# Kernel tuning notes

Hardware: AMD Instinct MI355X
Metric: run time of the kernel (lower is better)

Reference implementation:

```python
import jax, jax.numpy as jnp
import numpy as np

B, T, D, K = 64, 4096, 90, 32
LOG2PI = 1.8378770664093453


def setup_inputs() -> dict:
    key = jax.random.key(0)
    k1, k2, k3, k4, k5 = jax.random.split(key, 5)
    X = jax.random.normal(k1, (B, T, D), dtype=jnp.float32)
    state_priors = jax.random.uniform(k2, (K,), dtype=jnp.float32)
    transition_matrix = jax.random.uniform(k3, (K, K), dtype=jnp.float32)
    mu = jax.random.normal(k4, (K, D), dtype=jnp.float32) * 0.5
    log_var = jax.random.normal(k5, (K, D), dtype=jnp.float32) * 0.1
    return {"X": X, "state_priors": state_priors,
            "transition_matrix": transition_matrix, "mu": mu, "log_var": log_var}


def _emission_logprobs(X, mu, log_var):
    # Diagonal-Gaussian log density per state: (B,T,K)
    # expand (x-mu)^2*inv_var to avoid materializing a (B,T,K,D) tensor
    inv_var = jnp.exp(-log_var)                                   # (K,D)
    quad = (jnp.einsum('btd,kd->btk', X * X, inv_var)
            - 2.0 * jnp.einsum('btd,kd->btk', X, mu * inv_var)
            + jnp.sum(mu * mu * inv_var, axis=-1))                # (B,T,K)
    return -0.5 * (quad + jnp.sum(log_var, axis=-1) + D * LOG2PI)


def reference(X, state_priors, transition_matrix, mu, log_var):
    log_A = jax.nn.log_softmax(transition_matrix, axis=1)   # (K,K)
    log_pi = jax.nn.log_softmax(state_priors, axis=0)       # (K,)
    em = _emission_logprobs(X, mu, log_var)                 # (B,T,K)

    log_alpha0 = log_pi + em[:, 0, :]                       # (B,K)

    def step(log_alpha, e_t):
        # log_alpha: (B,K), e_t: (B,K)
        la = e_t + jax.nn.logsumexp(log_alpha[:, :, None] + log_A[None], axis=1)
        return la, None

    em_rest = jnp.swapaxes(em[:, 1:, :], 0, 1)              # (T-1,B,K)
    log_alpha_T, _ = jax.lax.scan(step, log_alpha0, em_rest)
    # sum over subjects of logsumexp over states at final timestep
    return jnp.sum(jax.nn.logsumexp(log_alpha_T, axis=-1))
```

## Files before the change

kernel.cpp:

```cpp
#include <hip/hip_runtime.h>
#include <stdint.h>

#define B_ 64
#define T_ 4096
#define D_ 90
#define K_ 32
#define CH_ 32
#define F_  128
#define NB_ 2048

typedef float f32x16 __attribute__((ext_vector_type(16)));
typedef float f32x2  __attribute__((ext_vector_type(2)));
typedef __bf16 bf16x8 __attribute__((ext_vector_type(8)));

#define WS_A     0
#define WS_PI    1024
#define WS_C0    1056
#define WS_WF    1088
#define WS_EACC  4160
#define WS_MS    12352
#define WS_E0    20544
#define WS_Q2    22080

#define LDS_WREG(w) ((w) * 1280)
#define LDS_WF      5120
#define LDS_TOT     11264

__device__ __forceinline__ int perm_r(int r) {
  int t2 = (r >> 2) & 3;
  return r + ((t2 == 1) ? 4 : (t2 == 2) ? -4 : 0);
}
__device__ __forceinline__ uint32_t pk2(float hi, float lo) {
  return __builtin_amdgcn_perm(__float_as_uint(hi), __float_as_uint(lo), 0x07060302u);
}
__device__ __forceinline__ uint32_t rnd_pk(float hi, float lo) {
  uint32_t uh = __float_as_uint(hi) + 0x8000u;
  uint32_t ul = __float_as_uint(lo) + 0x8000u;
  return __builtin_amdgcn_perm(uh, ul, 0x07060302u);
}
__device__ __forceinline__ float bf2f(ushort u) {
  return __uint_as_float(((uint32_t)u) << 16);
}
__device__ __forceinline__ bf16x8 mkbf(uint32_t a, uint32_t b, uint32_t c, uint32_t d) {
  union { uint32_t u[4]; bf16x8 v; } x;
  x.u[0] = a; x.u[1] = b; x.u[2] = c; x.u[3] = d;
  return x.v;
}

__global__ __launch_bounds__(1024) void prep_kernel(
    const float* __restrict__ priors, const float* __restrict__ trans,
    const float* __restrict__ mu, const float* __restrict__ lv,
    float* __restrict__ ws) {
  int tid = threadIdx.x;
  {
    float v = trans[tid];
    float m = v;
    #pragma unroll
    for (int mk = 16; mk; mk >>= 1) m = fmaxf(m, __shfl_xor(m, mk));
    float e = expf(v - m);
    float s = e;
    #pragma unroll
    for (int mk = 16; mk; mk >>= 1) s += __shfl_xor(s, mk);
    ws[WS_A + tid] = e / s;
  }
  if (tid < 32) {
    float v = priors[tid];
    float m = v;
    #pragma unroll
    for (int mk = 16; mk; mk >>= 1) m = fmaxf(m, __shfl_xor(m, mk));
    float e = expf(v - m);
    float s = e;
    #pragma unroll
    for (int mk = 16; mk; mk >>= 1) s += __shfl_xor(s, mk);
    ws[WS_PI + tid] = e / s;
  }
  for (int i = tid; i < 6144; i += 1024) {
    int j = i & 7, l = (i >> 3) & 63, cm = i >> 9;
    int c = cm >> 1, mat = cm & 1;
    int h = l >> 5, nn = l & 31;
    int d = 16 * c + 8 * h + j;
    float v = 0.0f;
    if (d < D_) {
      float ivd = expf(-lv[nn * D_ + d]);
      v = (mat == 0) ? -0.5f * ivd : mu[nn * D_ + d] * ivd;
    }
    ((ushort*)(ws + WS_WF))[i] = (ushort)((__float_as_uint(v) + 0x8000u) >> 16);
  }
  {
    int nn = tid >> 5, j = tid & 31;
    float s = 0.0f;
    for (int d = j; d < D_; d += 32) {
      float lvv = lv[nn * D_ + d];
      float iv  = expf(-lvv);
      float m_  = mu[nn * D_ + d];
      s += m_ * m_ * iv + lvv;
    }
    #pragma unroll
    for (int mk = 16; mk; mk >>= 1) s += __shfl_xor(s, mk);
    if (j == 0) ws[WS_C0 + nn] = -0.5f * (s + (float)D_ * 1.8378770664093453f);
  }
}

__global__ __launch_bounds__(256, 7) void fused_kernel(const float* __restrict__ X,
                                                       float* __restrict__ ws,
                                                       float* __restrict__ out) {
  __shared__ __align__(16) ushort sh[LDS_TOT];
  __shared__ float msb[4];
  __shared__ int   peb[4];
  int tid = threadIdx.x;
  int l = tid & 63, w = tid >> 6;
  int n = l & 31, h = l >> 5;
  int tB = blockIdx.x << 7;
  int t0 = tB + (w << 5);
  int b  = t0 >> 12;
  if (blockIdx.x == 0 && tid == 0) *out = 0.0f;

  {
    const uint4* wfp = (const uint4*)((const ushort*)(ws + WS_WF));
    uint4* wfl = (uint4*)(sh + LDS_WF);
    #pragma unroll
    for (int k = 0; k < 3; ++k) wfl[tid + (k << 8)] = wfp[tid + (k << 8)];
  }
  float c0 = ws[WS_C0 + n];

  int srow = l >> 1, sp = l & 1;
  const float* xg = X + (size_t)(t0 + srow) * D_ + 8 * sp;
  ushort* xbuf = sh + LDS_WREG(w);
  float2 va[4];
  auto xload = [&](int c) {
    #pragma unroll
    for (int s = 0; s < 4; ++s) {
      int d = 16 * c + 8 * sp + 2 * s;
      if (d < D_) va[s] = *(const float2*)(xg + 16 * c + 2 * s);
      else { va[s].x = 0.0f; va[s].y = 0.0f; }
    }
  };
  auto xwrite = [&]() {
    uint4 pkv;
    pkv.x = rnd_pk(va[0].y, va[0].x);
    pkv.y = rnd_pk(va[1].y, va[1].x);
    pkv.z = rnd_pk(va[2].y, va[2].x);
    pkv.w = rnd_pk(va[3].y, va[3].x);
    *(uint4*)(xbuf + srow * 24 + 8 * sp) = pkv;
  };
  xload(0);
  xwrite();
  xload(1);
  __syncthreads();

  const ushort* wfl = sh + LDS_WF;
  f32x16 acc;
  #pragma unroll
  for (int r = 0; r < 16; ++r) acc[r] = 0.0f;
  #pragma unroll
  for (int c = 0; c < 6; ++c) {
    union { uint4 u; bf16x8 v; } xb;
    xb.u = *(const uint4*)(xbuf + n * 24 + 8 * h);
    float x[8];
    #pragma unroll
    for (int j = 0; j < 8; ++j) {
      uint32_t uu = ((const uint32_t*)&xb.u)[j >> 1];
      x[j] = bf2f((j & 1) ? (ushort)(uu >> 16) : (ushort)(uu & 0xFFFF));
    }
    union { uint32_t u[4]; bf16x8 v; } x2b;
    #pragma unroll
    for (int r = 0; r < 4; ++r) {
      f32x2 xv = { x[2*r], x[2*r+1] };
      f32x2 xs = xv * xv;
      x2b.u[r] = rnd_pk(xs[1], xs[0]);
    }
    union { uint4 u; bf16x8 v; } w1, w2;
    w2.u = *(const uint4*)(wfl + (2 * c)     * 512 + l * 8);
    w1.u = *(const uint4*)(wfl + (2 * c + 1) * 512 + l * 8);
    acc = __builtin_amdgcn_mfma_f32_32x32x16_bf16(xb.v,  w1.v, acc, 0, 0, 0);
    acc = __builtin_amdgcn_mfma_f32_32x32x16_bf16(x2b.v, w2.v, acc, 0, 0, 0);
    if (c < 5) {
      xwrite();
      if (c < 4) xload(c + 2);
    }
  }
  float em[16], mrow[16];
  #pragma unroll
  for (int r = 0; r < 16; ++r) {
    float v = acc[r] + c0;
    em[r] = v;
    float m = v;
    #pragma unroll
    for (int mk = 1; mk <= 16; mk <<= 1) m = fmaxf(m, __shfl_xor(m, mk));
    mrow[r] = m;
  }
  ushort* Ew = sh + LDS_WREG(w);
  #pragma unroll
  for (int q = 0; q < 4; ++q) {
    float e0 = exp2f((em[4*q]   - mrow[4*q])   * 1.44269504088896f);
    float e1 = exp2f((em[4*q+1] - mrow[4*q+1]) * 1.44269504088896f);
    float e2 = exp2f((em[4*q+2] - mrow[4*q+2]) * 1.44269504088896f);
    float e3 = exp2f((em[4*q+3] - mrow[4*q+3]) * 1.44269504088896f);
    uint2 d;
    d.x = rnd_pk(e1, e0);
    d.y = rnd_pk(e3, e2);
    *(uint2*)(Ew + n * 40 + 8 * q + 4 * h) = d;
    if (q == 0 && h == 0 && (t0 & (T_ - 1)) == 0)
      ((ushort*)(ws + WS_E0))[b * K_ + n] = (ushort)(d.x & 0xFFFF);
  }
  float msum = 0.0f;
  #pragma unroll
  for (int r = 0; r < 16; ++r) msum += mrow[r];
  msum += __shfl_xor(msum, 32);
  if (l == 0) msb[w] = msum;

  int col = perm_r(n);
  const float* A = ws + WS_A;
  f32x2 astat2[8];
  #pragma unroll
  for (int r = 0; r < 4; ++r) {
    astat2[r]     = f32x2{ A[(8 * h + 2 * r) * K_ + col],
                           A[(8 * h + 2 * r + 1) * K_ + col] };
    astat2[4 + r] = f32x2{ A[(16 + 8 * h + 2 * r) * K_ + col],
                           A[(16 + 8 * h + 2 * r + 1) * K_ + col] };
  }
  uint32_t q[8];
  #pragma unroll
  for (int r = 0; r < 4; ++r) {
    int s0 = 8 * h + 2 * r;
    uint32_t lo = (s0 == n)     ? 0x3F80u : 0u;
    uint32_t hi = (s0 + 1 == n) ? 0x3F80u : 0u;
    q[r] = lo | (hi << 16);
    int s2 = s0 + 16;
    lo = (s2 == n)     ? 0x3F80u : 0u;
    hi = (s2 + 1 == n) ? 0x3F80u : 0u;
    q[4 + r] = lo | (hi << 16);
  }
  int eacc = 0;
  const f32x16 z = {0.f,0.f,0.f,0.f,0.f,0.f,0.f,0.f,0.f,0.f,0.f,0.f,0.f,0.f,0.f,0.f};
  #pragma unroll
  for (int r = 0; r < 16; ++r) acc[r] = 0.0f;

  auto step = [&](float e0) {
    uint32_t au[8];
    #pragma unroll
    for (int r = 0; r < 4; ++r) {
      f32x2 p0 = astat2[r] * e0;
      f32x2 p1 = astat2[4 + r] * e0;
      au[r]     = pk2(p0[1], p0[0]);
      au[4 + r] = pk2(p1[1], p1[0]);
    }
    bf16x8 alo = mkbf(au[0], au[1], au[2], au[3]);
    bf16x8 ahi = mkbf(au[4], au[5], au[6], au[7]);
    bf16x8 qlo = mkbf(q[0], q[1], q[2], q[3]);
    bf16x8 qhi = mkbf(q[4], q[5], q[6], q[7]);
    acc = __builtin_amdgcn_mfma_f32_32x32x16_bf16(alo, qlo, z, 0, 0, 0);
    acc = __builtin_amdgcn_mfma_f32_32x32x16_bf16(ahi, qhi, acc, 0, 0, 0);
    #pragma unroll
    for (int r = 0; r < 4; ++r) {
      q[r]     = pk2(acc[2 * r + 1], acc[2 * r]);
      q[4 + r] = pk2(acc[8 + 2 * r + 1], acc[8 + 2 * r]);
    }
  };
  auto lmul = [&](uint4 lo, uint4 hi) {
    bf16x8 alo = mkbf(lo.x, lo.y, lo.z, lo.w);
    bf16x8 ahi = mkbf(hi.x, hi.y, hi.z, hi.w);
    bf16x8 qlo = mkbf(q[0], q[1], q[2], q[3]);
    bf16x8 qhi = mkbf(q[4], q[5], q[6], q[7]);
    acc = __builtin_amdgcn_mfma_f32_32x32x16_bf16(alo, qlo, z, 0, 0, 0);
    acc = __builtin_amdgcn_mfma_f32_32x32x16_bf16(ahi, qhi, acc, 0, 0, 0);
    #pragma unroll
    for (int r = 0; r < 4; ++r) {
      q[r]     = pk2(acc[2 * r + 1], acc[2 * r]);
      q[4 + r] = pk2(acc[8 + 2 * r + 1], acc[8 + 2 * r]);
    }
  };
  auto renorm = [&]() {
    float m = acc[0];
    #pragma unroll
    for (int r = 1; r < 16; ++r) m = fmaxf(m, acc[r]);
    #pragma unroll
    for (int mk = 1; mk <= 32; mk <<= 1) m = fmaxf(m, __shfl_xor(m, mk));
    int ex;
    frexpf(m, &ex);
    float sc = ldexpf(1.0f, -ex);
    eacc += ex;
    #pragma unroll
    for (int r = 0; r < 16; ++r) acc[r] *= sc;
    #pragma unroll
    for (int r = 0; r < 4; ++r) {
      q[r]     = pk2(acc[2 * r + 1], acc[2 * r]);
      q[4 + r] = pk2(acc[8 + 2 * r + 1], acc[8 + 2 * r]);
    }
  };

  const ushort* Eb = sh + LDS_WREG(w) + col * 40;
  int g0 = 0;
  if ((t0 & (T_ - 1)) == 0) {
    uint4 ev = *(const uint4*)(Eb);
    #pragma unroll
    for (int j = 1; j < 8; ++j) {
      uint32_t u = ((const uint32_t*)&ev)[j >> 1];
      step(bf2f((j & 1) ? (ushort)(u >> 16) : (ushort)(u & 0xFFFF)));
    }
    renorm();
    g0 = 1;
  }
  for (int g = g0; g < CH_ / 8; ++g) {
    uint4 ev = *(const uint4*)(Eb + 8 * g);
    #pragma unroll
    for (int j = 0; j < 8; ++j) {
      uint32_t u = ((const uint32_t*)&ev)[j >> 1];
      step(bf2f((j & 1) ? (ushort)(u >> 16) : (ushort)(u & 0xFFFF)));
    }
    renorm();
  }

  ushort* Qw = sh + LDS_WREG(w);
  #pragma unroll
  for (int r = 0; r < 16; ++r) {
    int m_ = (r & 3) + 8 * (r >> 2) + 4 * h;
    Qw[perm_r(m_) * 40 + n] = (ushort)(__float_as_uint(acc[r]) >> 16);
  }
  if (l == 0) peb[w] = eacc;
  __syncthreads();
  if (w != 0) return;

  #pragma unroll
  for (int r = 0; r < 4; ++r) {
    int s0 = 8 * h + 2 * r;
    uint32_t lo = (s0 == n)     ? 0x3F80u : 0u;
    uint32_t hi = (s0 + 1 == n) ? 0x3F80u : 0u;
    q[r] = lo | (hi << 16);
    int s2 = s0 + 16;
    lo = (s2 == n)     ? 0x3F80u : 0u;
    hi = (s2 + 1 == n) ? 0x3F80u : 0u;
    q[4 + r] = lo | (hi << 16);
  }
  eacc = peb[0] + peb[1] + peb[2] + peb[3];
  float msm = msb[0] + msb[1] + msb[2] + msb[3];
  #pragma unroll
  for (int r = 0; r < 16; ++r) acc[r] = 0.0f;
  #pragma unroll
  for (int p = 0; p < 4; ++p) {
    const ushort* base = sh + LDS_WREG(p) + col * 40;
    uint4 lo = *(const uint4*)(base + 8 * h);
    uint4 hi = *(const uint4*)(base + 16 + 8 * h);
    lmul(lo, hi);
  }
  renorm();
  ushort* Qo = (ushort*)(ws + WS_Q2) + (size_t)blockIdx.x * (K_ * K_);
  #pragma unroll
  for (int r = 0; r < 16; ++r) {
    int m_ = (r & 3) + 8 * (r >> 2) + 4 * h;
    Qo[perm_r(m_) * K_ + n] = (ushort)(__float_as_uint(acc[r]) >> 16);
  }
  if (l == 0) {
    ((int*)ws)[WS_EACC + blockIdx.x] = eacc;
    ws[WS_MS + blockIdx.x] = msm;
  }
}

__global__ __launch_bounds__(256) void combine_kernel(float* __restrict__ ws,
                                                      float* __restrict__ out) {
  __shared__ __align__(16) ushort pm[4][1280];
  __shared__ int pe[4];
  int tid = threadIdx.x;
  int l = tid & 63, w = tid >> 6;
  int h = l >> 5, n = l & 31;
  int b = blockIdx.x;
  int row = perm_r(n);
  int eacc;
  {
    const int* ea = ((const int*)ws) + WS_EACC + b * 32 + w * 8;
    int v = (l < 8) ? ea[l] : 0;
    #pragma unroll
    for (int mk = 1; mk <= 4; mk <<= 1) v += __shfl_xor(v, mk);
    eacc = __shfl(v, 0);
  }
  uint32_t q[8];
  #pragma unroll
  for (int r = 0; r < 4; ++r) {
    int s0 = 8 * h + 2 * r;
    uint32_t lo = (s0 == n)     ? 0x3F80u : 0u;
    uint32_t hi = (s0 + 1 == n) ? 0x3F80u : 0u;
    q[r] = lo | (hi << 16);
    int s2 = s0 + 16;
    lo = (s2 == n)     ? 0x3F80u : 0u;
    hi = (s2 + 1 == n) ? 0x3F80u : 0u;
    q[4 + r] = lo | (hi << 16);
  }
  f32x16 acc;
  #pragma unroll
  for (int r = 0; r < 16; ++r) acc[r] = 0.0f;
  const f32x16 z = {0.f,0.f,0.f,0.f,0.f,0.f,0.f,0.f,0.f,0.f,0.f,0.f,0.f,0.f,0.f,0.f};

  auto lmul = [&](uint4 lo, uint4 hi) {
    bf16x8 alo = mkbf(lo.x, lo.y, lo.z, lo.w);
    bf16x8 ahi = mkbf(hi.x, hi.y, hi.z, hi.w);
    bf16x8 qlo = mkbf(q[0], q[1], q[2], q[3]);
    bf16x8 qhi = mkbf(q[4], q[5], q[6], q[7]);
    acc = __builtin_amdgcn_mfma_f32_32x32x16_bf16(alo, qlo, z, 0, 0, 0);
    acc = __builtin_amdgcn_mfma_f32_32x32x16_bf16(ahi, qhi, acc, 0, 0, 0);
    #pragma unroll
    for (int r = 0; r < 4; ++r) {
      q[r]     = pk2(acc[2 * r + 1], acc[2 * r]);
      q[4 + r] = pk2(acc[8 + 2 * r + 1], acc[8 + 2 * r]);
    }
  };
  auto renorm = [&]() {
    float m = acc[0];
    #pragma unroll
    for (int r = 1; r < 16; ++r) m = fmaxf(m, acc[r]);
    #pragma unroll
    for (int mk = 1; mk <= 32; mk <<= 1) m = fmaxf(m, __shfl_xor(m, mk));
    int ex;
    frexpf(m, &ex);
    float sc = ldexpf(1.0f, -ex);
    eacc += ex;
    #pragma unroll
    for (int r = 0; r < 16; ++r) acc[r] *= sc;
    #pragma unroll
    for (int r = 0; r < 4; ++r) {
      q[r]     = pk2(acc[2 * r + 1], acc[2 * r]);
      q[4 + r] = pk2(acc[8 + 2 * r + 1], acc[8 + 2 * r]);
    }
  };

  const ushort* Qb = (const ushort*)(ws + WS_Q2) + (size_t)(b * 32 + w * 8) * (K_ * K_);
  #pragma unroll
  for (int p = 0; p < 8; ++p) {
    const ushort* Mc = Qb + (size_t)p * (K_ * K_) + row * K_;
    uint4 lo = *(const uint4*)(Mc + 8 * h);
    uint4 hi = *(const uint4*)(Mc + 16 + 8 * h);
    lmul(lo, hi);
    if ((p & 3) == 3) renorm();
  }
  #pragma unroll
  for (int r = 0; r < 16; ++r) {
    int m_ = (r & 3) + 8 * (r >> 2) + 4 * h;
    pm[w][perm_r(m_) * 40 + n] = (ushort)(__float_as_uint(acc[r]) >> 16);
  }
  if (l == 0) pe[w] = eacc;
  __syncthreads();
  if (w != 0) return;

  float alpha0 = ws[WS_PI + n] * bf2f(((const ushort*)(ws + WS_E0))[b * K_ + n]);
  float msm;
  {
    float v = (l < 32) ? ws[WS_MS + b * 32 + l] : 0.0f;
    #pragma unroll
    for (int mk = 1; mk <= 32; mk <<= 1) v += __shfl_xor(v, mk);
    msm = v;
  }
  #pragma unroll
  for (int r = 0; r < 4; ++r) {
    int s0 = 8 * h + 2 * r;
    uint32_t lo = (s0 == n)     ? 0x3F80u : 0u;
    uint32_t hi = (s0 + 1 == n) ? 0x3F80u : 0u;
    q[r] = lo | (hi << 16);
    int s2 = s0 + 16;
    lo = (s2 == n)     ? 0x3F80u : 0u;
    hi = (s2 + 1 == n) ? 0x3F80u : 0u;
    q[4 + r] = lo | (hi << 16);
  }
  #pragma unroll
  for (int r = 0; r < 16; ++r) acc[r] = 0.0f;
  int et = pe[0] + pe[1] + pe[2] + pe[3];
  #pragma unroll
  for (int p = 0; p < 4; ++p) {
    const ushort* base = pm[p] + row * 40;
    uint4 lo = *(const uint4*)(base + 8 * h);
    uint4 hi = *(const uint4*)(base + 16 + 8 * h);
    lmul(lo, hi);
  }
  float part = 0.0f;
  #pragma unroll
  for (int r = 0; r < 16; ++r) part += acc[r];
  part *= alpha0;
  #pragma unroll
  for (int mk = 1; mk <= 32; mk <<= 1) part += __shfl_xor(part, mk);
  if (l == 0) {
    float res = logf(part) + (float)et * 0.69314718055994531f + msm;
    atomicAdd(out, res);
  }
}

extern "C" void kernel_launch(void* const* d_in, const int* in_sizes, int n_in,
                              void* d_out, int out_size, void* d_ws, size_t ws_size,
                              hipStream_t stream) {
  (void)in_sizes; (void)n_in; (void)out_size; (void)ws_size;
  const float* X      = (const float*)d_in[0];
  const float* priors = (const float*)d_in[1];
  const float* trans  = (const float*)d_in[2];
  const float* mu     = (const float*)d_in[3];
  const float* lv     = (const float*)d_in[4];
  float* ws  = (float*)d_ws;
  float* out = (float*)d_out;
  prep_kernel<<<1, 1024, 0, stream>>>(priors, trans, mu, lv, ws);
  fused_kernel<<<NB_, 256, 0, stream>>>(X, ws, out);
  combine_kernel<<<B_, 256, 0, stream>>>(ws, out);
}
```

Before: 175.3 us.

## Split each wave's chunk scan into two interleaved independent MFMA chains

Each wave's 32-step transfer-matrix product is split into two independent 16-step chains (A and B) that are interleaved, so consecutive MFMAs of one chain can hide the dependent latency of the other. The two partial products are then combined through LDS with one extra matrix multiply and renormalisation. This doubles the accumulator and q registers, so the occupancy hint is lowered from 7 to 6 waves per SIMD. The extra combine step and the reduced occupancy are the costs traded for more instruction-level parallelism.

```diff
diff --git a/kernel.cpp b/kernel.cpp
--- a/kernel.cpp
+++ b/kernel.cpp
@@ -101,7 +101,7 @@
   }
 }
 
-__global__ __launch_bounds__(256, 7) void fused_kernel(const float* __restrict__ X,
+__global__ __launch_bounds__(256, 6) void fused_kernel(const float* __restrict__ X,
                                                        float* __restrict__ ws,
                                                        float* __restrict__ out) {
   __shared__ __align__(16) ushort sh[LDS_TOT];
@@ -219,24 +219,25 @@
     astat2[4 + r] = f32x2{ A[(16 + 8 * h + 2 * r) * K_ + col],
                            A[(16 + 8 * h + 2 * r + 1) * K_ + col] };
   }
-  uint32_t q[8];
+  int eacc = 0;
+  const f32x16 z = {0.f,0.f,0.f,0.f,0.f,0.f,0.f,0.f,0.f,0.f,0.f,0.f,0.f,0.f,0.f,0.f};
+  f32x16 accA, accB;
+  uint32_t qA[8], qB[8];
+  #pragma unroll
+  for (int r = 0; r < 16; ++r) { accA[r] = 0.0f; accB[r] = 0.0f; }
   #pragma unroll
   for (int r = 0; r < 4; ++r) {
     int s0 = 8 * h + 2 * r;
     uint32_t lo = (s0 == n)     ? 0x3F80u : 0u;
     uint32_t hi = (s0 + 1 == n) ? 0x3F80u : 0u;
-    q[r] = lo | (hi << 16);
+    qA[r] = lo | (hi << 16);  qB[r] = qA[r];
     int s2 = s0 + 16;
     lo = (s2 == n)     ? 0x3F80u : 0u;
     hi = (s2 + 1 == n) ? 0x3F80u : 0u;
-    q[4 + r] = lo | (hi << 16);
-  }
-  int eacc = 0;
-  const f32x16 z = {0.f,0.f,0.f,0.f,0.f,0.f,0.f,0.f,0.f,0.f,0.f,0.f,0.f,0.f,0.f,0.f};
-  #pragma unroll
-  for (int r = 0; r < 16; ++r) acc[r] = 0.0f;
-
-  auto step = [&](float e0) {
+    qA[4 + r] = lo | (hi << 16);  qB[4 + r] = qA[4 + r];
+  }
+
+  auto stepc = [&](f32x16& acc_, uint32_t (&q_)[8], float e0) {
     uint32_t au[8];
     #pragma unroll
     for (int r = 0; r < 4; ++r) {
@@ -247,33 +248,33 @@
     }
     bf16x8 alo = mkbf(au[0], au[1], au[2], au[3]);
     bf16x8 ahi = mkbf(au[4], au[5], au[6], au[7]);
-    bf16x8 qlo = mkbf(q[0], q[1], q[2], q[3]);
-    bf16x8 qhi = mkbf(q[4], q[5], q[6], q[7]);
-    acc = __builtin_amdgcn_mfma_f32_32x32x16_bf16(alo, qlo, z, 0, 0, 0);
-    acc = __builtin_amdgcn_mfma_f32_32x32x16_bf16(ahi, qhi, acc, 0, 0, 0);
-    #pragma unroll
-    for (int r = 0; r < 4; ++r) {
-      q[r]     = pk2(acc[2 * r + 1], acc[2 * r]);
-      q[4 + r] = pk2(acc[8 + 2 * r + 1], acc[8 + 2 * r]);
-    }
-  };
-  auto lmul = [&](uint4 lo, uint4 hi) {
+    bf16x8 qlo = mkbf(q_[0], q_[1], q_[2], q_[3]);
+    bf16x8 qhi = mkbf(q_[4], q_[5], q_[6], q_[7]);
+    acc_ = __builtin_amdgcn_mfma_f32_32x32x16_bf16(alo, qlo, z, 0, 0, 0);
+    acc_ = __builtin_amdgcn_mfma_f32_32x32x16_bf16(ahi, qhi, acc_, 0, 0, 0);
+    #pragma unroll
+    for (int r = 0; r < 4; ++r) {
+      q_[r]     = pk2(acc_[2 * r + 1], acc_[2 * r]);
+      q_[4 + r] = pk2(acc_[8 + 2 * r + 1], acc_[8 + 2 * r]);
+    }
+  };
+  auto lmulc = [&](f32x16& acc_, uint32_t (&q_)[8], uint4 lo, uint4 hi) {
     bf16x8 alo = mkbf(lo.x, lo.y, lo.z, lo.w);
     bf16x8 ahi = mkbf(hi.x, hi.y, hi.z, hi.w);
-    bf16x8 qlo = mkbf(q[0], q[1], q[2], q[3]);
-    bf16x8 qhi = mkbf(q[4], q[5], q[6], q[7]);
-    acc = __builtin_amdgcn_mfma_f32_32x32x16_bf16(alo, qlo, z, 0, 0, 0);
-    acc = __builtin_amdgcn_mfma_f32_32x32x16_bf16(ahi, qhi, acc, 0, 0, 0);
-    #pragma unroll
-    for (int r = 0; r < 4; ++r) {
-      q[r]     = pk2(acc[2 * r + 1], acc[2 * r]);
-      q[4 + r] = pk2(acc[8 + 2 * r + 1], acc[8 + 2 * r]);
-    }
-  };
-  auto renorm = [&]() {
-    float m = acc[0];
-    #pragma unroll
-    for (int r = 1; r < 16; ++r) m = fmaxf(m, acc[r]);
+    bf16x8 qlo = mkbf(q_[0], q_[1], q_[2], q_[3]);
+    bf16x8 qhi = mkbf(q_[4], q_[5], q_[6], q_[7]);
+    acc_ = __builtin_amdgcn_mfma_f32_32x32x16_bf16(alo, qlo, z, 0, 0, 0);
+    acc_ = __builtin_amdgcn_mfma_f32_32x32x16_bf16(ahi, qhi, acc_, 0, 0, 0);
+    #pragma unroll
+    for (int r = 0; r < 4; ++r) {
+      q_[r]     = pk2(acc_[2 * r + 1], acc_[2 * r]);
+      q_[4 + r] = pk2(acc_[8 + 2 * r + 1], acc_[8 + 2 * r]);
+    }
+  };
+  auto renormc = [&](f32x16& acc_, uint32_t (&q_)[8]) {
+    float m = acc_[0];
+    #pragma unroll
+    for (int r = 1; r < 16; ++r) m = fmaxf(m, acc_[r]);
     #pragma unroll
     for (int mk = 1; mk <= 32; mk <<= 1) m = fmaxf(m, __shfl_xor(m, mk));
     int ex;
@@ -281,41 +282,55 @@
     float sc = ldexpf(1.0f, -ex);
     eacc += ex;
     #pragma unroll
-    for (int r = 0; r < 16; ++r) acc[r] *= sc;
-    #pragma unroll
-    for (int r = 0; r < 4; ++r) {
-      q[r]     = pk2(acc[2 * r + 1], acc[2 * r]);
-      q[4 + r] = pk2(acc[8 + 2 * r + 1], acc[8 + 2 * r]);
+    for (int r = 0; r < 16; ++r) acc_[r] *= sc;
+    #pragma unroll
+    for (int r = 0; r < 4; ++r) {
+      q_[r]     = pk2(acc_[2 * r + 1], acc_[2 * r]);
+      q_[4 + r] = pk2(acc_[8 + 2 * r + 1], acc_[8 + 2 * r]);
     }
   };
 
   const ushort* Eb = sh + LDS_WREG(w) + col * 40;
-  int g0 = 0;
-  if ((t0 & (T_ - 1)) == 0) {
-    uint4 ev = *(const uint4*)(Eb);
-    #pragma unroll
-    for (int j = 1; j < 8; ++j) {
-      uint32_t u = ((const uint32_t*)&ev)[j >> 1];
-      step(bf2f((j & 1) ? (ushort)(u >> 16) : (ushort)(u & 0xFFFF)));
-    }
-    renorm();
-    g0 = 1;
-  }
-  for (int g = g0; g < CH_ / 8; ++g) {
-    uint4 ev = *(const uint4*)(Eb + 8 * g);
+  bool first = ((t0 & (T_ - 1)) == 0);
+  #pragma unroll
+  for (int g = 0; g < 2; ++g) {
+    uint4 evA = *(const uint4*)(Eb + 8 * g);
+    uint4 evB = *(const uint4*)(Eb + 8 * (g + 2));
     #pragma unroll
     for (int j = 0; j < 8; ++j) {
-      uint32_t u = ((const uint32_t*)&ev)[j >> 1];
-      step(bf2f((j & 1) ? (ushort)(u >> 16) : (ushort)(u & 0xFFFF)));
-    }
-    renorm();
+      uint32_t uA = ((const uint32_t*)&evA)[j >> 1];
+      uint32_t uB = ((const uint32_t*)&evB)[j >> 1];
+      float eA = bf2f((j & 1) ? (ushort)(uA >> 16) : (ushort)(uA & 0xFFFF));
+      float eB = bf2f((j & 1) ? (ushort)(uB >> 16) : (ushort)(uB & 0xFFFF));
+      if (g == 0 && j == 0) {
+        if (!first) stepc(accA, qA, eA);
+      } else {
+        stepc(accA, qA, eA);
+      }
+      stepc(accB, qB, eB);
+    }
+    renormc(accA, qA);
+    renormc(accB, qB);
   }
 
   ushort* Qw = sh + LDS_WREG(w);
   #pragma unroll
   for (int r = 0; r < 16; ++r) {
     int m_ = (r & 3) + 8 * (r >> 2) + 4 * h;
-    Qw[perm_r(m_) * 40 + n] = (ushort)(__float_as_uint(acc[r]) >> 16);
+    Qw[perm_r(m_) * 40 + n] = (ushort)(__float_as_uint(accB[r]) >> 16);
+  }
+  {
+    const ushort* baseB = sh + LDS_WREG(w) + col * 40;
+    uint4 lo = *(const uint4*)(baseB + 8 * h);
+    uint4 hi = *(const uint4*)(baseB + 16 + 8 * h);
+    lmulc(accA, qA, lo, hi);
+  }
+  renormc(accA, qA);
+
+  #pragma unroll
+  for (int r = 0; r < 16; ++r) {
+    int m_ = (r & 3) + 8 * (r >> 2) + 4 * h;
+    Qw[perm_r(m_) * 40 + n] = (ushort)(__float_as_uint(accA[r]) >> 16);
   }
   if (l == 0) peb[w] = eacc;
   __syncthreads();
@@ -326,29 +341,29 @@
     int s0 = 8 * h + 2 * r;
     uint32_t lo = (s0 == n)     ? 0x3F80u : 0u;
     uint32_t hi = (s0 + 1 == n) ? 0x3F80u : 0u;
-    q[r] = lo | (hi << 16);
+    qA[r] = lo | (hi << 16);
     int s2 = s0 + 16;
     lo = (s2 == n)     ? 0x3F80u : 0u;
     hi = (s2 + 1 == n) ? 0x3F80u : 0u;
-    q[4 + r] = lo | (hi << 16);
+    qA[4 + r] = lo | (hi << 16);
   }
   eacc = peb[0] + peb[1] + peb[2] + peb[3];
   float msm = msb[0] + msb[1] + msb[2] + msb[3];
   #pragma unroll
-  for (int r = 0; r < 16; ++r) acc[r] = 0.0f;
+  for (int r = 0; r < 16; ++r) accA[r] = 0.0f;
   #pragma unroll
   for (int p = 0; p < 4; ++p) {
     const ushort* base = sh + LDS_WREG(p) + col * 40;
     uint4 lo = *(const uint4*)(base + 8 * h);
     uint4 hi = *(const uint4*)(base + 16 + 8 * h);
-    lmul(lo, hi);
-  }
-  renorm();
+    lmulc(accA, qA, lo, hi);
+  }
+  renormc(accA, qA);
   ushort* Qo = (ushort*)(ws + WS_Q2) + (size_t)blockIdx.x * (K_ * K_);
   #pragma unroll
   for (int r = 0; r < 16; ++r) {
     int m_ = (r & 3) + 8 * (r >> 2) + 4 * h;
-    Qo[perm_r(m_) * K_ + n] = (ushort)(__float_as_uint(acc[r]) >> 16);
+    Qo[perm_r(m_) * K_ + n] = (ushort)(__float_as_uint(accA[r]) >> 16);
   }
   if (l == 0) {
     ((int*)ws)[WS_EACC + blockIdx.x] = eacc;
```

Measured after the change: 178.4 us. No clear change (+1.8%).
